# Kernel optimization log

Measured on AMD Instinct MI355X. Metric: run time of the kernel, lower is better.

The kernel has to match this reference:

```python
import jax, jax.numpy as jnp
import numpy as np

N = 100000      # nodes
E = 1600000     # edges (avg degree 16)
D_IN = 128
D_H = 128
D_OUT = 64


def setup_inputs() -> dict:
    key = jax.random.key(0)
    ks = jax.random.split(key, 8)
    x = jax.random.normal(ks[0], (N, D_IN), dtype=jnp.float32)
    edge_index = jax.random.randint(ks[1], (2, E), 0, N, dtype=jnp.int64)
    # PyG GraphConv params: lin_rel (with bias) applied to aggregated messages,
    # lin_root (no bias) applied to self features. Kaiming-ish init scale.
    s1 = 1.0 / np.sqrt(D_IN)
    s2 = 1.0 / np.sqrt(D_H)
    W_rel1 = jax.random.uniform(ks[2], (D_H, D_IN), jnp.float32, -s1, s1)
    b_rel1 = jax.random.uniform(ks[3], (D_H,), jnp.float32, -s1, s1)
    W_root1 = jax.random.uniform(ks[4], (D_H, D_IN), jnp.float32, -s1, s1)
    W_rel2 = jax.random.uniform(ks[5], (D_OUT, D_H), jnp.float32, -s2, s2)
    b_rel2 = jax.random.uniform(ks[6], (D_OUT,), jnp.float32, -s2, s2)
    W_root2 = jax.random.uniform(ks[7], (D_OUT, D_H), jnp.float32, -s2, s2)
    return {
        "x": x, "edge_index": edge_index,
        "W_rel1": W_rel1, "b_rel1": b_rel1, "W_root1": W_root1,
        "W_rel2": W_rel2, "b_rel2": b_rel2, "W_root2": W_root2,
    }


def _graph_conv(x, src, dst, W_rel, b_rel, W_root):
    # sum-aggregate neighbor features x[src] into destination nodes,
    # then out = lin_rel(agg) + lin_root(x)  (PyG GraphConv, aggr='add')
    agg = jax.ops.segment_sum(x[src], dst, num_segments=x.shape[0])  # [N, d_in]
    return agg @ W_rel.T + b_rel + x @ W_root.T                      # [N, d_out]


def reference(x, edge_index, W_rel1, b_rel1, W_root1, W_rel2, b_rel2, W_root2):
    src, dst = edge_index[0], edge_index[1]
    h = jax.nn.relu(_graph_conv(x, src, dst, W_rel1, b_rel1, W_root1))  # [N, D_H]
    out = _graph_conv(h, src, dst, W_rel2, b_rel2, W_root2)             # [N, D_OUT]
    # reshape(-1, 1, output_dim) + cat over relations (relations == 1)
    return out.reshape(-1, 1, D_OUT)
```

## Files before the change

kernel.cpp:

```cpp
#include <hip/hip_runtime.h>
#include <hip/hip_bf16.h>


#define NPASS 8
#define FILL_GRID 2048

typedef unsigned short ushort_t;
using bfrag = __attribute__((ext_vector_type(8))) short;
using f32x4 = __attribute__((ext_vector_type(4))) float;

__device__ __forceinline__ ushort_t f2bf(float f) {
    unsigned int u = __float_as_uint(f);
    unsigned int r = (u + 0x7fff + ((u >> 16) & 1)) >> 16;
    return (ushort_t)r;
}

__device__ __forceinline__ float bf2f(ushort_t v) {
    return __uint_as_float(((unsigned int)v) << 16);
}

__device__ __forceinline__ void bf2x(unsigned int v, float& lo, float& hi) {
    lo = __uint_as_float(v << 16);
    hi = __uint_as_float(v & 0xffff0000u);
}

__device__ __forceinline__ int4 ldnt_int4(const int* p) {
    unsigned long long a = __builtin_nontemporal_load((const unsigned long long*)p);
    unsigned long long b = __builtin_nontemporal_load(((const unsigned long long*)p) + 1);
    int4 r;
    r.x = (int)(unsigned int)(a & 0xffffffffull);
    r.y = (int)(unsigned int)(a >> 32);
    r.z = (int)(unsigned int)(b & 0xffffffffull);
    r.w = (int)(unsigned int)(b >> 32);
    return r;
}


__global__ __launch_bounds__(256) void hist_kernel(const int* __restrict__ dst,
                                                   int* __restrict__ deg, int E, int N) {
    const int pass = blockIdx.x & (NPASS - 1);
    const int chunk = blockIdx.x >> 3;
    const int rangeSize = (N + NPASS - 1) / NPASS;
    const int lo = pass * rangeSize;
    const int hi = (lo + rangeSize < N) ? lo + rangeSize : N;
    const int base = chunk * 1024 + threadIdx.x * 4;
    if (base + 3 < E) {
        const int4 d4 = ldnt_int4(dst + base);
        if (d4.x >= lo && d4.x < hi) atomicAdd(&deg[d4.x], 1);
        if (d4.y >= lo && d4.y < hi) atomicAdd(&deg[d4.y], 1);
        if (d4.z >= lo && d4.z < hi) atomicAdd(&deg[d4.z], 1);
        if (d4.w >= lo && d4.w < hi) atomicAdd(&deg[d4.w], 1);
    } else {
        for (int i = 0; i < 4; ++i) {
            int e = base + i;
            if (e < E) {
                int d = dst[e];
                if (d >= lo && d < hi) atomicAdd(&deg[d], 1);
            }
        }
    }
}

__global__ __launch_bounds__(256) void scan1_kernel(const int* __restrict__ deg,
                                                    int* __restrict__ bsum, int N) {
    int t = threadIdx.x;
    int base = blockIdx.x * 1024 + t * 4;
    int s = 0;
    if (base + 3 < N) {
        int4 v = *(const int4*)(deg + base);
        s = v.x + v.y + v.z + v.w;
    } else {
#pragma unroll
        for (int i = 0; i < 4; ++i)
            if (base + i < N) s += deg[base + i];
    }
#pragma unroll
    for (int d = 32; d > 0; d >>= 1) s += __shfl_down(s, d);
    __shared__ int wsum[4];
    int lane = t & 63, w = t >> 6;
    if (lane == 0) wsum[w] = s;
    __syncthreads();
    if (t == 0) bsum[blockIdx.x] = wsum[0] + wsum[1] + wsum[2] + wsum[3];
}

__global__ __launch_bounds__(256) void scan2_kernel(const int* __restrict__ bsum,
                                                    int* __restrict__ boff,
                                                    int* __restrict__ offN, int B) {
    __shared__ int s[256];
    int t = threadIdx.x;
    int v = (t < B) ? bsum[t] : 0;
    s[t] = v;
    __syncthreads();
    for (int d = 1; d < 256; d <<= 1) {
        int u = (t >= d) ? s[t - d] : 0;
        __syncthreads();
        s[t] += u;
        __syncthreads();
    }
    if (t < B) boff[t] = s[t] - v;
    if (t == B - 1) *offN = s[t];
}

__global__ __launch_bounds__(256) void scan3_kernel(const int* __restrict__ deg,
                                                    const int* __restrict__ boff,
                                                    int* __restrict__ off,
                                                    int* __restrict__ cursor, int N) {
    int t = threadIdx.x;
    int base = blockIdx.x * 1024 + t * 4;
    int d0 = 0, d1 = 0, d2 = 0, d3 = 0;
    if (base + 3 < N) {
        int4 v = *(const int4*)(deg + base);
        d0 = v.x; d1 = v.y; d2 = v.z; d3 = v.w;
    } else {
        if (base + 0 < N) d0 = deg[base + 0];
        if (base + 1 < N) d1 = deg[base + 1];
        if (base + 2 < N) d2 = deg[base + 2];
    }
    int s = d0 + d1 + d2 + d3;
    int lane = t & 63, w = t >> 6;
    int incl = s;
#pragma unroll
    for (int d = 1; d < 64; d <<= 1) {
        int u = __shfl_up(incl, d);
        if (lane >= d) incl += u;
    }
    __shared__ int wsum[4];
    if (lane == 63) wsum[w] = incl;
    __syncthreads();
    int wpre = 0;
#pragma unroll
    for (int i = 0; i < 3; ++i)
        if (i < w) wpre += wsum[i];
    int excl = incl - s + wpre + boff[blockIdx.x];
    int e0 = excl, e1 = e0 + d0, e2 = e1 + d1, e3 = e2 + d2;
    if (base + 3 < N) {
        *(int4*)(off + base) = make_int4(e0, e1, e2, e3);
        *(int4*)(cursor + base) = make_int4(e0, e1, e2, e3);
    } else {
        if (base + 0 < N) { off[base + 0] = e0; cursor[base + 0] = e0; }
        if (base + 1 < N) { off[base + 1] = e1; cursor[base + 1] = e1; }
        if (base + 2 < N) { off[base + 2] = e2; cursor[base + 2] = e2; }
    }
}

__global__ __launch_bounds__(256) void fill_kernel(const int* __restrict__ src,
                                                   const int* __restrict__ dst,
                                                   int* __restrict__ cursor,
                                                   int* __restrict__ csr, int E, int N) {
    const int pass = blockIdx.x & (NPASS - 1);
    const int rangeSize = (N + NPASS - 1) / NPASS;
    const int lo = pass * rangeSize;
    const int hi = (lo + rangeSize < N) ? lo + rangeSize : N;
    const int nChunk = (E + 1023) >> 10;
    for (int chunk = blockIdx.x >> 3; chunk < nChunk; chunk += FILL_GRID / NPASS) {
        const int base = chunk * 1024 + threadIdx.x * 4;
        if (base + 3 < E) {
            const int4 s4 = ldnt_int4(src + base);
            const int4 d4 = ldnt_int4(dst + base);
            if (d4.x >= lo && d4.x < hi) csr[atomicAdd(&cursor[d4.x], 1)] = s4.x;
            if (d4.y >= lo && d4.y < hi) csr[atomicAdd(&cursor[d4.y], 1)] = s4.y;
            if (d4.z >= lo && d4.z < hi) csr[atomicAdd(&cursor[d4.z], 1)] = s4.z;
            if (d4.w >= lo && d4.w < hi) csr[atomicAdd(&cursor[d4.w], 1)] = s4.w;
        } else {
            for (int i = 0; i < 4; ++i) {
                int e = base + i;
                if (e < E) {
                    int d = dst[e];
                    if (d >= lo && d < hi) csr[atomicAdd(&cursor[d], 1)] = src[e];
                }
            }
        }
    }
}


__global__ __launch_bounds__(256) void cvt_kernel(const float* __restrict__ in,
                                                  ushort_t* __restrict__ out, int n) {
    int base = (blockIdx.x * 256 + threadIdx.x) * 4;
    if (base + 3 < n) {
        float4 v = *(const float4*)(in + base);
        ushort4 o;
        o.x = f2bf(v.x); o.y = f2bf(v.y); o.z = f2bf(v.z); o.w = f2bf(v.w);
        *(ushort4*)(out + base) = o;
    } else {
        for (int i = 0; i < 4 && base + i < n; ++i) out[base + i] = f2bf(in[base + i]);
    }
}

__global__ __launch_bounds__(256) void cvt_w_kernel(const float* __restrict__ Wr1,
                                                    const float* __restrict__ Wo1,
                                                    const float* __restrict__ Wr2,
                                                    const float* __restrict__ Wo2,
                                                    ushort_t* __restrict__ wcat1,
                                                    ushort_t* __restrict__ wcat2) {
    int i = blockIdx.x * 256 + threadIdx.x;
    if (i < 16384) wcat1[i] = f2bf(Wr1[i]);
    else if (i < 32768) wcat1[i] = f2bf(Wo1[i - 16384]);
    else if (i < 40960) wcat2[i - 32768] = f2bf(Wr2[i - 32768]);
    else if (i < 49152) wcat2[i - 32768] = f2bf(Wo2[i - 40960]);
}


template <int BN, int SPLIT, int O2F>
__global__ __launch_bounds__(256, 2)
void mfma_gemm(const ushort_t* __restrict__ A, const ushort_t* __restrict__ Wc,
               ushort_t* __restrict__ O1, void* __restrict__ O2v, int Nrows) {
    constexpr int NT = BN / 16;
    const int w = threadIdx.x >> 6;
    const int lane = threadIdx.x & 63;
    const int m0 = blockIdx.x * 64 + w * 16;
    const int lm = lane & 15;
    const int lk8 = (lane >> 4) * 8;

    f32x4 acc[NT];
#pragma unroll
    for (int t = 0; t < NT; ++t) {
        acc[t][0] = 0.f; acc[t][1] = 0.f; acc[t][2] = 0.f; acc[t][3] = 0.f;
    }

    int ar = m0 + lm;
    ar = ar < Nrows ? ar : Nrows - 1;
    const ushort_t* Arow = A + (size_t)ar * 128;

#pragma unroll
    for (int kk = 0; kk < 4; ++kk) {
        const bfrag af = *(const bfrag*)(Arow + kk * 32 + lk8);
#pragma unroll
        for (int t = 0; t < NT; ++t) {
            const bfrag bf = *(const bfrag*)(Wc + ((size_t)(t * 16 + lm) << 7) + kk * 32 + lk8);
            acc[t] = __builtin_amdgcn_mfma_f32_16x16x32_bf16(af, bf, acc[t], 0, 0, 0);
        }
    }

    const int rbase = m0 + (lane >> 4) * 4;
#pragma unroll
    for (int t = 0; t < NT; ++t) {
        const int col = t * 16 + lm;
#pragma unroll
        for (int r = 0; r < 4; ++r) {
            const int row = rbase + r;
            if (row >= Nrows) continue;
            const float v = acc[t][r];
            if (col < SPLIT) {
                O1[(size_t)row * SPLIT + col] = f2bf(v);
            } else {
                if (O2F) ((float*)O2v)[(size_t)row * (BN - SPLIT) + (col - SPLIT)] = v;
                else ((ushort_t*)O2v)[(size_t)row * (BN - SPLIT) + (col - SPLIT)] = f2bf(v);
            }
        }
    }
}


template <int D, int OB>
__global__ __launch_bounds__(256)
void agg_k(const ushort_t* __restrict__ F, const int* __restrict__ csr,
           const int* __restrict__ off, void* __restrict__ OUTv, int N) {
    constexpr int LPN = (D == 128) ? 32 : 16;
    constexpr int NPB = 256 / LPN;
    int n = blockIdx.x * NPB + (threadIdx.x / LPN);
    if (n >= N) return;
    int lane = threadIdx.x & (LPN - 1);
    int b = off[n], e = off[n + 1];
    const size_t col = (size_t)lane * 4;
    float a0 = 0.f, a1 = 0.f, a2 = 0.f, a3 = 0.f;
    int i = b;
    for (; i + 4 <= e; i += 4) {
        int s0 = csr[i], s1 = csr[i + 1], s2 = csr[i + 2], s3 = csr[i + 3];
        uint2 v0 = *(const uint2*)(F + (size_t)s0 * D + col);
        uint2 v1 = *(const uint2*)(F + (size_t)s1 * D + col);
        uint2 v2 = *(const uint2*)(F + (size_t)s2 * D + col);
        uint2 v3 = *(const uint2*)(F + (size_t)s3 * D + col);
        float l, h;
        bf2x(v0.x, l, h); a0 += l; a1 += h;
        bf2x(v0.y, l, h); a2 += l; a3 += h;
        bf2x(v1.x, l, h); a0 += l; a1 += h;
        bf2x(v1.y, l, h); a2 += l; a3 += h;
        bf2x(v2.x, l, h); a0 += l; a1 += h;
        bf2x(v2.y, l, h); a2 += l; a3 += h;
        bf2x(v3.x, l, h); a0 += l; a1 += h;
        bf2x(v3.y, l, h); a2 += l; a3 += h;
    }
    for (; i < e; ++i) {
        uint2 v = *(const uint2*)(F + (size_t)csr[i] * D + col);
        float l, h;
        bf2x(v.x, l, h); a0 += l; a1 += h;
        bf2x(v.y, l, h); a2 += l; a3 += h;
    }
    if (OB) {
        ushort_t* OUT = (ushort_t*)OUTv;
        ushort4 o;
        o.x = f2bf(a0); o.y = f2bf(a1); o.z = f2bf(a2); o.w = f2bf(a3);
        *(ushort4*)(OUT + (size_t)n * D + col) = o;
    } else {
        float* OUT = (float*)OUTv;
        float4 r; r.x = a0; r.y = a1; r.z = a2; r.w = a3;
        *(float4*)(OUT + (size_t)n * D + col) = r;
    }
}


__global__ __launch_bounds__(256) void epi1_kernel(const ushort_t* __restrict__ a1,
                                                   const ushort_t* __restrict__ hpre,
                                                   const float* __restrict__ b1,
                                                   ushort_t* __restrict__ h, int total) {
    int base = (blockIdx.x * 256 + threadIdx.x) * 8;
    if (base + 7 >= total) {
        for (int i = 0; i < 8 && base + i < total; ++i) {
            float v = bf2f(a1[base + i]) + b1[(base + i) & 127] + bf2f(hpre[base + i]);
            h[base + i] = f2bf(v > 0.f ? v : 0.f);
        }
        return;
    }
    uint4 av = *(const uint4*)(a1 + base);
    uint4 pv = *(const uint4*)(hpre + base);
    int c0 = base & 127;
    float4 bA = *(const float4*)(b1 + c0);
    float4 bB = *(const float4*)(b1 + c0 + 4);
    float bb[8] = {bA.x, bA.y, bA.z, bA.w, bB.x, bB.y, bB.z, bB.w};
    unsigned int aw[4] = {av.x, av.y, av.z, av.w};
    unsigned int pw[4] = {pv.x, pv.y, pv.z, pv.w};
    ushort4 o[2];
    ushort_t res[8];
#pragma unroll
    for (int q = 0; q < 4; ++q) {
        float al, ah, pl, ph;
        bf2x(aw[q], al, ah);
        bf2x(pw[q], pl, ph);
        float v0 = al + bb[q * 2 + 0] + pl;
        float v1 = ah + bb[q * 2 + 1] + ph;
        res[q * 2 + 0] = f2bf(v0 > 0.f ? v0 : 0.f);
        res[q * 2 + 1] = f2bf(v1 > 0.f ? v1 : 0.f);
    }
    o[0].x = res[0]; o[0].y = res[1]; o[0].z = res[2]; o[0].w = res[3];
    o[1].x = res[4]; o[1].y = res[5]; o[1].z = res[6]; o[1].w = res[7];
    *(ushort4*)(h + base) = o[0];
    *(ushort4*)(h + base + 4) = o[1];
}

__global__ __launch_bounds__(256) void epi2_kernel(const ushort_t* __restrict__ a2,
                                                   const float* __restrict__ opre,
                                                   const float* __restrict__ b2,
                                                   float* __restrict__ out, int total) {
    int base = (blockIdx.x * 256 + threadIdx.x) * 4;
    if (base + 3 >= total) {
        for (int i = 0; i < 4 && base + i < total; ++i)
            out[base + i] = bf2f(a2[base + i]) + b2[(base + i) & 63] + opre[base + i];
        return;
    }
    uint2 av = *(const uint2*)(a2 + base);
    float4 ov = *(const float4*)(opre + base);
    float4 bv = *(const float4*)(b2 + (base & 63));
    float al, ah, bl, bh;
    bf2x(av.x, al, ah);
    bf2x(av.y, bl, bh);
    float4 r;
    r.x = al + bv.x + ov.x;
    r.y = ah + bv.y + ov.y;
    r.z = bl + bv.z + ov.z;
    r.w = bh + bv.w + ov.w;
    *(float4*)(out + base) = r;
}

extern "C" void kernel_launch(void* const* d_in, const int* in_sizes, int n_in,
                              void* d_out, int out_size, void* d_ws, size_t ws_size,
                              hipStream_t stream) {
    const float* x   = (const float*)d_in[0];
    const int*   ei  = (const int*)d_in[1];
    const float* Wr1 = (const float*)d_in[2];
    const float* br1 = (const float*)d_in[3];
    const float* Wo1 = (const float*)d_in[4];
    const float* Wr2 = (const float*)d_in[5];
    const float* br2 = (const float*)d_in[6];
    const float* Wo2 = (const float*)d_in[7];
    float* out = (float*)d_out;

    const int N = in_sizes[0] / 128;
    const int E = in_sizes[1] / 2;

    const int* srcv = ei;
    const int* dstv = ei + E;

    ushort_t* bufA = (ushort_t*)d_ws;
    ushort_t* bufB = bufA + (size_t)N * 128;
    ushort_t* bufC = bufB + (size_t)N * 128;
    ushort_t* bufD = bufC + (size_t)N * 128;
    ushort_t* wcat1 = bufD + (size_t)N * 128;
    ushort_t* wcat2 = wcat1 + 256 * 128;
    int*      deg  = (int*)(wcat2 + 128 * 128);
    int*      off  = deg + N;
    int*      cur  = off + N + 8;
    int*      csr  = cur + N;
    int*      bsum = csr + E;
    int*      boff = bsum + 256;

    const int B = (N + 1023) / 1024;
    const int edgePassBlocks = ((E + 1023) / 1024) * NPASS;
    const int gemmBlocks = (N + 63) / 64;
    const int agg128Blocks = (N + 7) / 8;
    const int agg64Blocks = (N + 15) / 16;
    const int cvtXBlocks = (N * 128 / 4 + 255) / 256;
    const int epi1Blocks = (N * 128 / 8 + 255) / 256;
    const int epi2Blocks = (N * 64 / 4 + 255) / 256;

    hipMemsetAsync(deg, 0, (size_t)N * sizeof(int), stream);
    hist_kernel<<<edgePassBlocks, 256, 0, stream>>>(dstv, deg, E, N);
    scan1_kernel<<<B, 256, 0, stream>>>(deg, bsum, N);
    scan2_kernel<<<1, 256, 0, stream>>>(bsum, boff, off + N, B);
    scan3_kernel<<<B, 256, 0, stream>>>(deg, boff, off, cur, N);
    fill_kernel<<<FILL_GRID, 256, 0, stream>>>(srcv, dstv, cur, csr, E, N);

    cvt_kernel<<<cvtXBlocks, 256, 0, stream>>>(x, bufA , N * 128);
    cvt_w_kernel<<<192, 256, 0, stream>>>(Wr1, Wo1, Wr2, Wo2, wcat1, wcat2);

    mfma_gemm<256, 128, 0><<<gemmBlocks, 256, 0, stream>>>(bufA, wcat1, bufB ,
                                                           bufC , N);
    agg_k<128, 1><<<agg128Blocks, 256, 0, stream>>>(bufB, csr, off, bufD , N);
    epi1_kernel<<<epi1Blocks, 256, 0, stream>>>(bufD, bufC, br1, bufA , N * 128);

    mfma_gemm<128, 64, 1><<<gemmBlocks, 256, 0, stream>>>(bufA, wcat2, bufB ,
                                                          bufC , N);
    agg_k<64, 1><<<agg64Blocks, 256, 0, stream>>>(bufB, csr, off, bufD , N);
    epi2_kernel<<<epi2Blocks, 256, 0, stream>>>(bufD, (const float*)bufC, br2, out, N * 64);
}
```

Baseline: 473.2 us.

## Fuse x conversion into GEMM and epilogues into aggregation kernels

```diff
diff --git a/kernel.cpp b/kernel.cpp
--- a/kernel.cpp
+++ b/kernel.cpp
@@ -147,12 +147,12 @@
                                                    const int* __restrict__ dst,
                                                    int* __restrict__ cursor,
                                                    int* __restrict__ csr, int E, int N) {
-    const int pass = blockIdx.x & (NPASS - 1);
+    const int pass = blockIdx.x >> 8;
     const int rangeSize = (N + NPASS - 1) / NPASS;
     const int lo = pass * rangeSize;
     const int hi = (lo + rangeSize < N) ? lo + rangeSize : N;
     const int nChunk = (E + 1023) >> 10;
-    for (int chunk = blockIdx.x >> 3; chunk < nChunk; chunk += FILL_GRID / NPASS) {
+    for (int chunk = (blockIdx.x & 255); chunk < nChunk; chunk += FILL_GRID / NPASS) {
         const int base = chunk * 1024 + threadIdx.x * 4;
         if (base + 3 < E) {
             const int4 s4 = ldnt_int4(src + base);
@@ -173,20 +173,6 @@
     }
 }
 
-
-__global__ __launch_bounds__(256) void cvt_kernel(const float* __restrict__ in,
-                                                  ushort_t* __restrict__ out, int n) {
-    int base = (blockIdx.x * 256 + threadIdx.x) * 4;
-    if (base + 3 < n) {
-        float4 v = *(const float4*)(in + base);
-        ushort4 o;
-        o.x = f2bf(v.x); o.y = f2bf(v.y); o.z = f2bf(v.z); o.w = f2bf(v.w);
-        *(ushort4*)(out + base) = o;
-    } else {
-        for (int i = 0; i < 4 && base + i < n; ++i) out[base + i] = f2bf(in[base + i]);
-    }
-}
-
 __global__ __launch_bounds__(256) void cvt_w_kernel(const float* __restrict__ Wr1,
                                                     const float* __restrict__ Wo1,
                                                     const float* __restrict__ Wr2,
@@ -201,9 +187,9 @@
 }
 
 
-template <int BN, int SPLIT, int O2F>
+template <int BN, int SPLIT, int O2F, int AF>
 __global__ __launch_bounds__(256, 2)
-void mfma_gemm(const ushort_t* __restrict__ A, const ushort_t* __restrict__ Wc,
+void mfma_gemm(const void* __restrict__ Av, const ushort_t* __restrict__ Wc,
                ushort_t* __restrict__ O1, void* __restrict__ O2v, int Nrows) {
     constexpr int NT = BN / 16;
     const int w = threadIdx.x >> 6;
@@ -220,11 +206,22 @@
 
     int ar = m0 + lm;
     ar = ar < Nrows ? ar : Nrows - 1;
-    const ushort_t* Arow = A + (size_t)ar * 128;
 
 #pragma unroll
     for (int kk = 0; kk < 4; ++kk) {
-        const bfrag af = *(const bfrag*)(Arow + kk * 32 + lk8);
+        bfrag af;
+        if (AF) {
+            const float* Arow = ((const float*)Av) + (size_t)ar * 128;
+            const float4 fa = *(const float4*)(Arow + kk * 32 + lk8);
+            const float4 fb = *(const float4*)(Arow + kk * 32 + lk8 + 4);
+            af[0] = (short)f2bf(fa.x); af[1] = (short)f2bf(fa.y);
+            af[2] = (short)f2bf(fa.z); af[3] = (short)f2bf(fa.w);
+            af[4] = (short)f2bf(fb.x); af[5] = (short)f2bf(fb.y);
+            af[6] = (short)f2bf(fb.z); af[7] = (short)f2bf(fb.w);
+        } else {
+            const ushort_t* Arow = ((const ushort_t*)Av) + (size_t)ar * 128;
+            af = *(const bfrag*)(Arow + kk * 32 + lk8);
+        }
 #pragma unroll
         for (int t = 0; t < NT; ++t) {
             const bfrag bf = *(const bfrag*)(Wc + ((size_t)(t * 16 + lm) << 7) + kk * 32 + lk8);
@@ -252,10 +249,11 @@
 }
 
 
-template <int D, int OB>
+template <int D, int MODE>
 __global__ __launch_bounds__(256)
 void agg_k(const ushort_t* __restrict__ F, const int* __restrict__ csr,
-           const int* __restrict__ off, void* __restrict__ OUTv, int N) {
+           const int* __restrict__ off, const void* __restrict__ PRE,
+           const float* __restrict__ bias, void* __restrict__ OUTv, int N) {
     constexpr int LPN = (D == 128) ? 32 : 16;
     constexpr int NPB = 256 / LPN;
     int n = blockIdx.x * NPB + (threadIdx.x / LPN);
@@ -287,79 +285,32 @@
         bf2x(v.x, l, h); a0 += l; a1 += h;
         bf2x(v.y, l, h); a2 += l; a3 += h;
     }
-    if (OB) {
-        ushort_t* OUT = (ushort_t*)OUTv;
+
+    const float4 bv = *(const float4*)(bias + col);
+    if (MODE == 1) {
+        uint2 pv = *(const uint2*)((const ushort_t*)PRE + (size_t)n * D + col);
+        float p0, p1, p2, p3;
+        bf2x(pv.x, p0, p1);
+        bf2x(pv.y, p2, p3);
+        float v0 = a0 + bv.x + p0;
+        float v1 = a1 + bv.y + p1;
+        float v2 = a2 + bv.z + p2;
+        float v3 = a3 + bv.w + p3;
         ushort4 o;
-        o.x = f2bf(a0); o.y = f2bf(a1); o.z = f2bf(a2); o.w = f2bf(a3);
-        *(ushort4*)(OUT + (size_t)n * D + col) = o;
-    } else {
-        float* OUT = (float*)OUTv;
-        float4 r; r.x = a0; r.y = a1; r.z = a2; r.w = a3;
-        *(float4*)(OUT + (size_t)n * D + col) = r;
-    }
-}
-
-
-__global__ __launch_bounds__(256) void epi1_kernel(const ushort_t* __restrict__ a1,
-                                                   const ushort_t* __restrict__ hpre,
-                                                   const float* __restrict__ b1,
-                                                   ushort_t* __restrict__ h, int total) {
-    int base = (blockIdx.x * 256 + threadIdx.x) * 8;
-    if (base + 7 >= total) {
-        for (int i = 0; i < 8 && base + i < total; ++i) {
-            float v = bf2f(a1[base + i]) + b1[(base + i) & 127] + bf2f(hpre[base + i]);
-            h[base + i] = f2bf(v > 0.f ? v : 0.f);
-        }
-        return;
-    }
-    uint4 av = *(const uint4*)(a1 + base);
-    uint4 pv = *(const uint4*)(hpre + base);
-    int c0 = base & 127;
-    float4 bA = *(const float4*)(b1 + c0);
-    float4 bB = *(const float4*)(b1 + c0 + 4);
-    float bb[8] = {bA.x, bA.y, bA.z, bA.w, bB.x, bB.y, bB.z, bB.w};
-    unsigned int aw[4] = {av.x, av.y, av.z, av.w};
-    unsigned int pw[4] = {pv.x, pv.y, pv.z, pv.w};
-    ushort4 o[2];
-    ushort_t res[8];
-#pragma unroll
-    for (int q = 0; q < 4; ++q) {
-        float al, ah, pl, ph;
-        bf2x(aw[q], al, ah);
-        bf2x(pw[q], pl, ph);
-        float v0 = al + bb[q * 2 + 0] + pl;
-        float v1 = ah + bb[q * 2 + 1] + ph;
-        res[q * 2 + 0] = f2bf(v0 > 0.f ? v0 : 0.f);
-        res[q * 2 + 1] = f2bf(v1 > 0.f ? v1 : 0.f);
-    }
-    o[0].x = res[0]; o[0].y = res[1]; o[0].z = res[2]; o[0].w = res[3];
-    o[1].x = res[4]; o[1].y = res[5]; o[1].z = res[6]; o[1].w = res[7];
-    *(ushort4*)(h + base) = o[0];
-    *(ushort4*)(h + base + 4) = o[1];
-}
-
-__global__ __launch_bounds__(256) void epi2_kernel(const ushort_t* __restrict__ a2,
-                                                   const float* __restrict__ opre,
-                                                   const float* __restrict__ b2,
-                                                   float* __restrict__ out, int total) {
-    int base = (blockIdx.x * 256 + threadIdx.x) * 4;
-    if (base + 3 >= total) {
-        for (int i = 0; i < 4 && base + i < total; ++i)
-            out[base + i] = bf2f(a2[base + i]) + b2[(base + i) & 63] + opre[base + i];
-        return;
-    }
-    uint2 av = *(const uint2*)(a2 + base);
-    float4 ov = *(const float4*)(opre + base);
-    float4 bv = *(const float4*)(b2 + (base & 63));
-    float al, ah, bl, bh;
-    bf2x(av.x, al, ah);
-    bf2x(av.y, bl, bh);
-    float4 r;
-    r.x = al + bv.x + ov.x;
-    r.y = ah + bv.y + ov.y;
-    r.z = bl + bv.z + ov.z;
-    r.w = bh + bv.w + ov.w;
-    *(float4*)(out + base) = r;
+        o.x = f2bf(v0 > 0.f ? v0 : 0.f);
+        o.y = f2bf(v1 > 0.f ? v1 : 0.f);
+        o.z = f2bf(v2 > 0.f ? v2 : 0.f);
+        o.w = f2bf(v3 > 0.f ? v3 : 0.f);
+        *(ushort4*)((ushort_t*)OUTv + (size_t)n * D + col) = o;
+    } else {
+        float4 ov = *(const float4*)((const float*)PRE + (size_t)n * D + col);
+        float4 r;
+        r.x = a0 + bv.x + ov.x;
+        r.y = a1 + bv.y + ov.y;
+        r.z = a2 + bv.z + ov.z;
+        r.w = a3 + bv.w + ov.w;
+        *(float4*)((float*)OUTv + (size_t)n * D + col) = r;
+    }
 }
 
 extern "C" void kernel_launch(void* const* d_in, const int* in_sizes, int n_in,
@@ -381,11 +332,10 @@
     const int* srcv = ei;
     const int* dstv = ei + E;
 
-    ushort_t* bufA = (ushort_t*)d_ws;
-    ushort_t* bufB = bufA + (size_t)N * 128;
+    ushort_t* bufH = (ushort_t*)d_ws;
+    ushort_t* bufB = bufH + (size_t)N * 128;
     ushort_t* bufC = bufB + (size_t)N * 128;
-    ushort_t* bufD = bufC + (size_t)N * 128;
-    ushort_t* wcat1 = bufD + (size_t)N * 128;
+    ushort_t* wcat1 = bufC + (size_t)N * 128;
     ushort_t* wcat2 = wcat1 + 256 * 128;
     int*      deg  = (int*)(wcat2 + 128 * 128);
     int*      off  = deg + N;
@@ -399,9 +349,6 @@
     const int gemmBlocks = (N + 63) / 64;
     const int agg128Blocks = (N + 7) / 8;
     const int agg64Blocks = (N + 15) / 16;
-    const int cvtXBlocks = (N * 128 / 4 + 255) / 256;
-    const int epi1Blocks = (N * 128 / 8 + 255) / 256;
-    const int epi2Blocks = (N * 64 / 4 + 255) / 256;
 
     hipMemsetAsync(deg, 0, (size_t)N * sizeof(int), stream);
     hist_kernel<<<edgePassBlocks, 256, 0, stream>>>(dstv, deg, E, N);
@@ -410,16 +357,14 @@
     scan3_kernel<<<B, 256, 0, stream>>>(deg, boff, off, cur, N);
     fill_kernel<<<FILL_GRID, 256, 0, stream>>>(srcv, dstv, cur, csr, E, N);
 
-    cvt_kernel<<<cvtXBlocks, 256, 0, stream>>>(x, bufA , N * 128);
     cvt_w_kernel<<<192, 256, 0, stream>>>(Wr1, Wo1, Wr2, Wo2, wcat1, wcat2);
 
-    mfma_gemm<256, 128, 0><<<gemmBlocks, 256, 0, stream>>>(bufA, wcat1, bufB ,
-                                                           bufC , N);
-    agg_k<128, 1><<<agg128Blocks, 256, 0, stream>>>(bufB, csr, off, bufD , N);
-    epi1_kernel<<<epi1Blocks, 256, 0, stream>>>(bufD, bufC, br1, bufA , N * 128);
-
-    mfma_gemm<128, 64, 1><<<gemmBlocks, 256, 0, stream>>>(bufA, wcat2, bufB ,
-                                                          bufC , N);
-    agg_k<64, 1><<<agg64Blocks, 256, 0, stream>>>(bufB, csr, off, bufD , N);
-    epi2_kernel<<<epi2Blocks, 256, 0, stream>>>(bufD, (const float*)bufC, br2, out, N * 64);
-}
+    mfma_gemm<256, 128, 0, 1><<<gemmBlocks, 256, 0, stream>>>(x, wcat1, bufB ,
+                                                              bufC , N);
+    agg_k<128, 1><<<agg128Blocks, 256, 0, stream>>>(bufB, csr, off, bufC, br1,
+                                                    bufH , N);
+
+    mfma_gemm<128, 64, 1, 0><<<gemmBlocks, 256, 0, stream>>>(bufH, wcat2, bufB ,
+                                                             bufC , N);
+    agg_k<64, 2><<<agg64Blocks, 256, 0, stream>>>(bufB, csr, off, bufC, br2, out, N);
+}
```

Result: faster. 456.1 us (-3.6%).
